# Kernel optimization log

Measured on AMD Instinct MI355X. Metric: run time of the kernel, lower is better.

The kernel has to match this reference:

```python
import jax, jax.numpy as jnp
import numpy as np


def setup_inputs() -> dict:
    key = jax.random.key(0)
    k1, k2, k3 = jax.random.split(key, 3)
    N, DIN, DOUT = 8192, 256, 256
    adjacency = jax.random.uniform(k1, (N, N), dtype=jnp.float32)
    input_feature = jax.random.normal(k2, (N, DIN), dtype=jnp.float32)
    weight = jax.random.normal(k3, (DIN, DOUT), dtype=jnp.float32) * (1.0 / np.sqrt(DIN))
    bias = jnp.zeros((DOUT,), dtype=jnp.float32)
    return {"adjacency": adjacency, "input_feature": input_feature,
            "weight": weight, "bias": bias, "l": 1}


def reference(adjacency, input_feature, weight, bias, l):
    # support = X @ W
    support = input_feature @ weight  # [N, DOUT]
    # A = adjacency + l*I ; degrees = rowsum(A) = rowsum(adjacency) + l
    deg = jnp.sum(adjacency, axis=1) + jnp.asarray(l, adjacency.dtype)  # [N]
    # D^{-1/2} with inf (from zero degree) replaced by 0
    d = jnp.where(deg > 0, deg ** -0.5, jnp.zeros_like(deg))  # [N]
    # D @ adjacency @ D  (row scale then col scale of the ORIGINAL adjacency,
    # self-loops only affect the degree, matching the torch code)
    norm_adj = adjacency * d[:, None] * d[None, :]  # [N, N]
    out = norm_adj @ support + bias  # [N, DOUT]
    return out
```

## Files before the change

kernel.cpp:

```cpp
#include <hip/hip_runtime.h>
#include <hip/hip_bf16.h>


typedef __attribute__((ext_vector_type(8))) short short8;
typedef __attribute__((ext_vector_type(4))) float f32x4;

#define NN 8192
#define DD 256

__device__ inline unsigned short f2bfu(float x) {
    unsigned int u = __builtin_bit_cast(unsigned int, x);
    u += 0x7fffu + ((u >> 16) & 1u);
    return (unsigned short)(u >> 16);
}
__device__ inline unsigned int f2bf2u(float x, float y) {
    return (unsigned int)f2bfu(x) | ((unsigned int)f2bfu(y) << 16);
}
__device__ inline short8 cvt8(float4 a, float4 b) {
    union { unsigned int i[4]; short8 s; } u;
    u.i[0] = f2bf2u(a.x, a.y);
    u.i[1] = f2bf2u(a.z, a.w);
    u.i[2] = f2bf2u(b.x, b.y);
    u.i[3] = f2bf2u(b.z, b.w);
    return u.s;
}

__global__ __launch_bounds__(256) void rowsum_kernel(const float* __restrict__ A,
                                                     const int* __restrict__ lp,
                                                     float* __restrict__ d) {
    const int row = blockIdx.x;
    const int t = threadIdx.x;
    const float4* Arow = (const float4*)(A + (size_t)row * NN);
    float s = 0.f;
#pragma unroll
    for (int it = 0; it < NN / 4 / 256; ++it) {
        float4 v = Arow[it * 256 + t];
        s += (v.x + v.y) + (v.z + v.w);
    }
#pragma unroll
    for (int off = 32; off > 0; off >>= 1) s += __shfl_down(s, off, 64);
    __shared__ float wsum[4];
    if ((t & 63) == 0) wsum[t >> 6] = s;
    __syncthreads();
    if (t == 0) {
        float deg = ((wsum[0] + wsum[1]) + (wsum[2] + wsum[3])) + (float)(*lp);
        d[row] = deg > 0.f ? rsqrtf(deg) : 0.f;
    }
}

__global__ __launch_bounds__(256) void wtrans_kernel(const float* __restrict__ W,
                                                     unsigned short* __restrict__ WT) {
    __shared__ unsigned short tile[64][65];
    const int tx = threadIdx.x & 63, ty = threadIdx.x >> 6;
    const int i0 = (blockIdx.x & 3) * 64;
    const int n0 = (blockIdx.x >> 2) * 64;
#pragma unroll
    for (int r = ty; r < 64; r += 4)
        tile[r][tx] = f2bfu(W[(size_t)(i0 + r) * DD + n0 + tx]);
    __syncthreads();
#pragma unroll
    for (int r = ty; r < 64; r += 4)
        WT[(size_t)(n0 + r) * DD + i0 + tx] = tile[tx][r];
}

__global__ __launch_bounds__(256) void support_kernel(const float* __restrict__ X,
                                                      const unsigned short* __restrict__ WT,
                                                      const float* __restrict__ d,
                                                      unsigned short* __restrict__ ST) {
    const int j0 = blockIdx.x * 16;
    const int lane = threadIdx.x & 63;
    const int w = threadIdx.x >> 6;
    const int q = lane >> 4;
    const int l15 = lane & 15;
    const int nb = w * 64;

    f32x4 acc[4];
#pragma unroll
    for (int b = 0; b < 4; ++b) acc[b] = (f32x4)(0.f);

    const float* Xbase = X + (size_t)(j0 + l15) * DD + q * 8;
    const unsigned short* Wbase = WT + (size_t)(nb + l15) * DD + q * 8;

#pragma unroll
    for (int k0 = 0; k0 < DD; k0 += 32) {
        const float4* p = (const float4*)(Xbase + k0);
        short8 afr = cvt8(p[0], p[1]);
        short8 bfr[4];
#pragma unroll
        for (int ni = 0; ni < 4; ++ni)
            bfr[ni] = *(const short8*)(Wbase + ni * 16 * DD + k0);
#pragma unroll
        for (int ni = 0; ni < 4; ++ni)
            acc[ni] = __builtin_amdgcn_mfma_f32_16x16x32_bf16(afr, bfr[ni], acc[ni], 0, 0, 0);
    }

    const int j0r = j0 + q * 4;
    float dj[4];
#pragma unroll
    for (int r = 0; r < 4; ++r) dj[r] = d[j0r + r];
#pragma unroll
    for (int ni = 0; ni < 4; ++ni) {
        const int n = nb + ni * 16 + l15;
        unsigned int lo = f2bf2u(acc[ni][0] * dj[0], acc[ni][1] * dj[1]);
        unsigned int hi = f2bf2u(acc[ni][2] * dj[2], acc[ni][3] * dj[3]);
        *(uint2*)(ST + (size_t)n * NN + j0r) = make_uint2(lo, hi);
    }
}

#define KCHUNK 2048
#define BK 64
#define NITER (KCHUNK / BK)
__global__ __launch_bounds__(256) void main_gemm(const float* __restrict__ A,
                                                 const unsigned short* __restrict__ ST,
                                                 const float* __restrict__ d,
                                                 const float* __restrict__ bias,
                                                 float* __restrict__ out) {
    __shared__ __align__(16) unsigned short Abuf[2][64][72];

    const int mt = blockIdx.x & 127;
    const int kc = blockIdx.x >> 7;
    const int m0 = mt * 64;
    const int kbeg = kc * KCHUNK;
    const int tid = threadIdx.x;
    const int lane = tid & 63;
    const int w = tid >> 6;
    const int q = lane >> 4;
    const int l15 = lane & 15;
    const int nb = w * 64;
    const int srow = tid >> 4;
    const int scol = (tid & 15) * 4;

    const float* Ast = A + (size_t)(m0 + srow) * NN + kbeg + scol;
    const unsigned short* Bptr = ST + (size_t)(nb + l15) * NN + kbeg + q * 8;

    f32x4 acc[4][4];
#pragma unroll
    for (int a = 0; a < 4; ++a)
#pragma unroll
        for (int b = 0; b < 4; ++b) acc[a][b] = (f32x4)(0.f);

    f32x4 r[2][4];
    short8 bfr[2][2][4];

#pragma unroll
    for (int p = 0; p < 4; ++p)
        r[0][p] = __builtin_nontemporal_load((const f32x4*)(Ast + (size_t)(p * 16) * NN));
#pragma unroll
    for (int p = 0; p < 4; ++p)
        r[1][p] = __builtin_nontemporal_load((const f32x4*)(Ast + (size_t)(p * 16) * NN + BK));
#pragma unroll
    for (int kk2 = 0; kk2 < 2; ++kk2)
#pragma unroll
        for (int ni = 0; ni < 4; ++ni)
            bfr[0][kk2][ni] = *(const short8*)(Bptr + (size_t)(ni * 16) * NN + kk2 * 32);
#pragma unroll
    for (int p = 0; p < 4; ++p) {
        f32x4 v = r[0][p];
        *(uint2*)&Abuf[0][srow + p * 16][scol] =
            make_uint2(f2bf2u(v[0], v[1]), f2bf2u(v[2], v[3]));
    }

#pragma unroll 2
    for (int it = 0; it < NITER; ++it) {
        const int buf = it & 1;
        __asm__ __volatile__("s_waitcnt lgkmcnt(0)\n\ts_barrier" ::: "memory");

        if (it + 1 < NITER) {
#pragma unroll
            for (int kk2 = 0; kk2 < 2; ++kk2)
#pragma unroll
                for (int ni = 0; ni < 4; ++ni)
                    bfr[buf ^ 1][kk2][ni] =
                        *(const short8*)(Bptr + (size_t)(ni * 16) * NN + (it + 1) * BK + kk2 * 32);
        }
        if (it + 2 < NITER) {
#pragma unroll
            for (int p = 0; p < 4; ++p)
                r[buf][p] = __builtin_nontemporal_load(
                    (const f32x4*)(Ast + (size_t)(p * 16) * NN + (it + 2) * BK));
        }
        if (it + 1 < NITER) {
#pragma unroll
            for (int p = 0; p < 4; ++p) {
                f32x4 v = r[buf ^ 1][p];
                *(uint2*)&Abuf[buf ^ 1][srow + p * 16][scol] =
                    make_uint2(f2bf2u(v[0], v[1]), f2bf2u(v[2], v[3]));
            }
        }
#pragma unroll
        for (int kk2 = 0; kk2 < 2; ++kk2) {
            short8 afr[4];
#pragma unroll
            for (int mi = 0; mi < 4; ++mi)
                afr[mi] = *(const short8*)&Abuf[buf][mi * 16 + l15][kk2 * 32 + q * 8];
#pragma unroll
            for (int mi = 0; mi < 4; ++mi)
#pragma unroll
                for (int ni = 0; ni < 4; ++ni)
                    acc[mi][ni] = __builtin_amdgcn_mfma_f32_16x16x32_bf16(
                        afr[mi], bfr[buf][kk2][ni], acc[mi][ni], 0, 0, 0);
        }
    }

#pragma unroll
    for (int mi = 0; mi < 4; ++mi) {
        const int r0 = m0 + mi * 16 + q * 4;
        float dm[4];
#pragma unroll
        for (int rr = 0; rr < 4; ++rr) dm[rr] = d[r0 + rr];
#pragma unroll
        for (int ni = 0; ni < 4; ++ni) {
            const int n = nb + ni * 16 + l15;
            const float bv = (kc == 0) ? bias[n] : 0.f;
#pragma unroll
            for (int rr = 0; rr < 4; ++rr) {
                float val = acc[mi][ni][rr] * dm[rr] + bv;
                unsafeAtomicAdd(out + (size_t)(r0 + rr) * DD + n, val);
            }
        }
    }
}

extern "C" void kernel_launch(void* const* d_in, const int* in_sizes, int n_in,
                              void* d_out, int out_size, void* d_ws, size_t ws_size,
                              hipStream_t stream) {
    const float* A = (const float*)d_in[0];
    const float* X = (const float*)d_in[1];
    const float* W = (const float*)d_in[2];
    const float* bias = (const float*)d_in[3];
    const int* lp = (const int*)d_in[4];
    float* out = (float*)d_out;

    float* d = (float*)d_ws;
    unsigned short* WT = (unsigned short*)((char*)d_ws + 32768);
    unsigned short* ST = (unsigned short*)((char*)d_ws + 32768 + 131072);

    (void)hipMemsetAsync(d_out, 0, (size_t)NN * DD * sizeof(float), stream);
    rowsum_kernel<<<NN, 256, 0, stream>>>(A, lp, d);
    wtrans_kernel<<<16, 256, 0, stream>>>(W, WT);
    support_kernel<<<NN / 16, 256, 0, stream>>>(X, WT, d, ST);
    main_gemm<<<128 * (NN / KCHUNK), 256, 0, stream>>>(A, ST, d, bias, out);
}
```

Before: 483.4 us.

## Pre-convert adjacency to tiled bf16 in rowsum pass and reduce split-K partials

The rowsum pass now also writes the adjacency as bf16 into a pre-tiled, XOR-swizzled layout. The main GEMM then streams half the bytes straight into LDS with global_load_lds, which removes the in-loop fp32 load, convert and LDS store. Atomic adds into the output are replaced by per-chunk partial buffers and a separate reduce kernel that applies the row scale and bias, which also drops the memset. The cost is an extra 128MB bf16 write plus readback and 32MB of partials, in exchange for fewer adjacency bytes read in the GEMM and no atomics.

Result: faster. 472.1 us (-2.3%).

```diff
diff --git a/kernel.cpp b/kernel.cpp
--- a/kernel.cpp
+++ b/kernel.cpp
@@ -1,5 +1,4 @@
 #include <hip/hip_runtime.h>
-#include <hip/hip_bf16.h>
 
 
 typedef __attribute__((ext_vector_type(8))) short short8;
@@ -7,6 +6,9 @@
 
 #define NN 8192
 #define DD 256
+#define KCHUNK 2048
+#define BK 64
+#define NITER (KCHUNK / BK)
 
 __device__ inline unsigned short f2bfu(float x) {
     unsigned int u = __builtin_bit_cast(unsigned int, x);
@@ -25,26 +27,42 @@
     return u.s;
 }
 
-__global__ __launch_bounds__(256) void rowsum_kernel(const float* __restrict__ A,
-                                                     const int* __restrict__ lp,
-                                                     float* __restrict__ d) {
-    const int row = blockIdx.x;
+__device__ inline void gload16(const void* g, void* l) {
+    __builtin_amdgcn_global_load_lds(
+        (const __attribute__((address_space(1))) unsigned int*)g,
+        (__attribute__((address_space(3))) unsigned int*)l, 16, 0, 0);
+}
+
+__global__ __launch_bounds__(256) void rowsum_conv(const float* __restrict__ A,
+                                                   const int* __restrict__ lp,
+                                                   float* __restrict__ d,
+                                                   unsigned short* __restrict__ Abf) {
     const int t = threadIdx.x;
-    const float4* Arow = (const float4*)(A + (size_t)row * NN);
-    float s = 0.f;
-#pragma unroll
-    for (int it = 0; it < NN / 4 / 256; ++it) {
-        float4 v = Arow[it * 256 + t];
-        s += (v.x + v.y) + (v.z + v.w);
-    }
-#pragma unroll
-    for (int off = 32; off > 0; off >>= 1) s += __shfl_down(s, off, 64);
-    __shared__ float wsum[4];
-    if ((t & 63) == 0) wsum[t >> 6] = s;
-    __syncthreads();
-    if (t == 0) {
-        float deg = ((wsum[0] + wsum[1]) + (wsum[2] + wsum[3])) + (float)(*lp);
-        d[row] = deg > 0.f ? rsqrtf(deg) : 0.f;
+    const int rl = t >> 4;
+    const int cg = t & 15;
+    const int i = blockIdx.x * 16 + rl;
+    const int ti = i >> 6;
+    const int rt = i & 63;
+    const int swz = (rt & 7) << 4;
+
+    const f32x4* Ar = (const f32x4*)(A + (size_t)i * NN);
+    char* tb = (char*)Abf + (size_t)ti * 128 * 8192 + rt * 128 + ((8 * cg) ^ swz);
+
+    float s0 = 0.f, s1 = 0.f;
+#pragma unroll 4
+    for (int k = 0; k < 128; ++k) {
+        f32x4 v = __builtin_nontemporal_load(Ar + cg + 16 * k);
+        s0 += v[0] + v[1];
+        s1 += v[2] + v[3];
+        *(uint2*)(tb + (size_t)k * 8192) =
+            make_uint2(f2bf2u(v[0], v[1]), f2bf2u(v[2], v[3]));
+    }
+    float s = s0 + s1;
+#pragma unroll
+    for (int off = 8; off > 0; off >>= 1) s += __shfl_down(s, off, 16);
+    if (cg == 0) {
+        float deg = s + (float)(*lp);
+        d[i] = deg > 0.f ? rsqrtf(deg) : 0.f;
     }
 }
 
@@ -107,31 +125,24 @@
     }
 }
 
-#define KCHUNK 2048
-#define BK 64
-#define NITER (KCHUNK / BK)
-__global__ __launch_bounds__(256) void main_gemm(const float* __restrict__ A,
+__global__ __launch_bounds__(256) void main_gemm(const unsigned short* __restrict__ Abf,
                                                  const unsigned short* __restrict__ ST,
-                                                 const float* __restrict__ d,
-                                                 const float* __restrict__ bias,
-                                                 float* __restrict__ out) {
-    __shared__ __align__(16) unsigned short Abuf[2][64][72];
+                                                 float* __restrict__ part) {
+    __shared__ __align__(16) unsigned short Abuf[2][4096];
 
     const int mt = blockIdx.x & 127;
     const int kc = blockIdx.x >> 7;
-    const int m0 = mt * 64;
-    const int kbeg = kc * KCHUNK;
     const int tid = threadIdx.x;
     const int lane = tid & 63;
     const int w = tid >> 6;
     const int q = lane >> 4;
     const int l15 = lane & 15;
     const int nb = w * 64;
-    const int srow = tid >> 4;
-    const int scol = (tid & 15) * 4;
-
-    const float* Ast = A + (size_t)(m0 + srow) * NN + kbeg + scol;
-    const unsigned short* Bptr = ST + (size_t)(nb + l15) * NN + kbeg + q * 8;
+    const int swz = (l15 & 7) << 4;
+
+    const char* Ag = (const char*)Abf + ((size_t)mt * 128 + kc * NITER) * 8192
+                     + w * 2048 + lane * 16;
+    const unsigned short* Bptr = ST + (size_t)(nb + l15) * NN + kc * KCHUNK + q * 8;
 
     f32x4 acc[4][4];
 #pragma unroll
@@ -139,60 +150,53 @@
 #pragma unroll
         for (int b = 0; b < 4; ++b) acc[a][b] = (f32x4)(0.f);
 
-    f32x4 r[2][4];
     short8 bfr[2][2][4];
 
-#pragma unroll
-    for (int p = 0; p < 4; ++p)
-        r[0][p] = __builtin_nontemporal_load((const f32x4*)(Ast + (size_t)(p * 16) * NN));
-#pragma unroll
-    for (int p = 0; p < 4; ++p)
-        r[1][p] = __builtin_nontemporal_load((const f32x4*)(Ast + (size_t)(p * 16) * NN + BK));
+    {
+        unsigned short* l0 = &Abuf[0][w * 1024];
+        gload16(Ag, l0);
+        gload16(Ag + 1024, l0 + 512);
+    }
+    __builtin_amdgcn_sched_barrier(0);
 #pragma unroll
     for (int kk2 = 0; kk2 < 2; ++kk2)
 #pragma unroll
         for (int ni = 0; ni < 4; ++ni)
             bfr[0][kk2][ni] = *(const short8*)(Bptr + (size_t)(ni * 16) * NN + kk2 * 32);
-#pragma unroll
-    for (int p = 0; p < 4; ++p) {
-        f32x4 v = r[0][p];
-        *(uint2*)&Abuf[0][srow + p * 16][scol] =
-            make_uint2(f2bf2u(v[0], v[1]), f2bf2u(v[2], v[3]));
-    }
+    __builtin_amdgcn_sched_barrier(0);
+
+    const char* Ab0 = (const char*)&Abuf[0][0] + l15 * 128;
+    const char* Ab1 = (const char*)&Abuf[1][0] + l15 * 128;
 
 #pragma unroll 2
     for (int it = 0; it < NITER; ++it) {
         const int buf = it & 1;
-        __asm__ __volatile__("s_waitcnt lgkmcnt(0)\n\ts_barrier" ::: "memory");
+        __asm__ __volatile__("s_waitcnt vmcnt(8)\n\ts_barrier" ::: "memory");
 
         if (it + 1 < NITER) {
+            const char* gn = Ag + (size_t)(it + 1) * 8192;
+            unsigned short* ln = &Abuf[buf ^ 1][w * 1024];
+            gload16(gn, ln);
+            gload16(gn + 1024, ln + 512);
+        }
+        __builtin_amdgcn_sched_barrier(0);
+        if (it + 1 < NITER) {
 #pragma unroll
             for (int kk2 = 0; kk2 < 2; ++kk2)
 #pragma unroll
                 for (int ni = 0; ni < 4; ++ni)
-                    bfr[buf ^ 1][kk2][ni] =
-                        *(const short8*)(Bptr + (size_t)(ni * 16) * NN + (it + 1) * BK + kk2 * 32);
-        }
-        if (it + 2 < NITER) {
-#pragma unroll
-            for (int p = 0; p < 4; ++p)
-                r[buf][p] = __builtin_nontemporal_load(
-                    (const f32x4*)(Ast + (size_t)(p * 16) * NN + (it + 2) * BK));
-        }
-        if (it + 1 < NITER) {
-#pragma unroll
-            for (int p = 0; p < 4; ++p) {
-                f32x4 v = r[buf ^ 1][p];
-                *(uint2*)&Abuf[buf ^ 1][srow + p * 16][scol] =
-                    make_uint2(f2bf2u(v[0], v[1]), f2bf2u(v[2], v[3]));
-            }
-        }
+                    bfr[buf ^ 1][kk2][ni] = *(const short8*)(
+                        Bptr + (size_t)(ni * 16) * NN + (it + 1) * BK + kk2 * 32);
+        }
+        __builtin_amdgcn_sched_barrier(0);
+
+        const char* Ab = buf ? Ab1 : Ab0;
 #pragma unroll
         for (int kk2 = 0; kk2 < 2; ++kk2) {
             short8 afr[4];
 #pragma unroll
             for (int mi = 0; mi < 4; ++mi)
-                afr[mi] = *(const short8*)&Abuf[buf][mi * 16 + l15][kk2 * 32 + q * 8];
+                afr[mi] = *(const short8*)(Ab + mi * 2048 + ((kk2 * 64 + q * 16) ^ swz));
 #pragma unroll
             for (int mi = 0; mi < 4; ++mi)
 #pragma unroll
@@ -202,23 +206,37 @@
         }
     }
 
+    float* P = part + (size_t)kc * NN * DD;
 #pragma unroll
     for (int mi = 0; mi < 4; ++mi) {
-        const int r0 = m0 + mi * 16 + q * 4;
-        float dm[4];
-#pragma unroll
-        for (int rr = 0; rr < 4; ++rr) dm[rr] = d[r0 + rr];
+        const int r0 = mt * 64 + mi * 16 + q * 4;
 #pragma unroll
         for (int ni = 0; ni < 4; ++ni) {
             const int n = nb + ni * 16 + l15;
-            const float bv = (kc == 0) ? bias[n] : 0.f;
-#pragma unroll
-            for (int rr = 0; rr < 4; ++rr) {
-                float val = acc[mi][ni][rr] * dm[rr] + bv;
-                unsafeAtomicAdd(out + (size_t)(r0 + rr) * DD + n, val);
-            }
-        }
-    }
+#pragma unroll
+            for (int rr = 0; rr < 4; ++rr)
+                P[(size_t)(r0 + rr) * DD + n] = acc[mi][ni][rr];
+        }
+    }
+}
+
+__global__ __launch_bounds__(256) void reduce_kernel(const float* __restrict__ part,
+                                                     const float* __restrict__ d,
+                                                     const float* __restrict__ bias,
+                                                     float* __restrict__ out) {
+    const int idx = blockIdx.x * 256 + threadIdx.x;
+    const int i = idx >> 6;
+    const int c4 = (idx & 63) << 2;
+    const size_t off = (size_t)i * DD + c4;
+    const size_t stride = (size_t)NN * DD;
+    f32x4 s = *(const f32x4*)(part + off);
+    s += *(const f32x4*)(part + stride + off);
+    s += *(const f32x4*)(part + 2 * stride + off);
+    s += *(const f32x4*)(part + 3 * stride + off);
+    const float di = d[i];
+    const f32x4 b = *(const f32x4*)(bias + c4);
+    s = s * di + b;
+    *(f32x4*)(out + off) = s;
 }
 
 extern "C" void kernel_launch(void* const* d_in, const int* in_sizes, int n_in,
@@ -234,10 +252,13 @@
     float* d = (float*)d_ws;
     unsigned short* WT = (unsigned short*)((char*)d_ws + 32768);
     unsigned short* ST = (unsigned short*)((char*)d_ws + 32768 + 131072);
-
-    (void)hipMemsetAsync(d_out, 0, (size_t)NN * DD * sizeof(float), stream);
-    rowsum_kernel<<<NN, 256, 0, stream>>>(A, lp, d);
+    float* part = (float*)((char*)d_ws + 4358144);
+    unsigned short* Abf = (unsigned short*)((char*)d_ws + 37912576);
+    (void)ws_size;
+
+    rowsum_conv<<<NN / 16, 256, 0, stream>>>(A, lp, d, Abf);
     wtrans_kernel<<<16, 256, 0, stream>>>(W, WT);
     support_kernel<<<NN / 16, 256, 0, stream>>>(X, WT, d, ST);
-    main_gemm<<<128 * (NN / KCHUNK), 256, 0, stream>>>(A, ST, d, bias, out);
-}
+    main_gemm<<<128 * (NN / KCHUNK), 256, 0, stream>>>(Abf, ST, part);
+    reduce_kernel<<<NN * DD / 4 / 256, 256, 0, stream>>>(part, d, bias, out);
+}
```
